# Kernel optimization log

Measured on AMD Instinct MI355X. Metric: run time of the kernel, lower is better.

Reference implementation:

```python
import jax, jax.numpy as jnp
import numpy as np

N_BITS = 8
OUTLIER_THRESHOLD = 3.0  # in units of per-token std
QMAX = 2.0 ** (N_BITS - 1) - 1.0  # 127 for int8
EPS = 1e-6


def setup_inputs() -> dict:
    key = jax.random.key(0)
    kx, kw, kb = jax.random.split(key, 3)
    B, S, D_in, D_out = 4, 4096, 2048, 2048
    x = jax.random.normal(kx, (B, S, D_in), dtype=jnp.float32)
    # nn.Linear default init scale ~ 1/sqrt(in_features)
    W = jax.random.normal(kw, (D_out, D_in), dtype=jnp.float32) / np.sqrt(D_in)
    b = jax.random.normal(kb, (D_out,), dtype=jnp.float32) / np.sqrt(D_in)
    return {"x": x, "W": W, "b": b}


def _dynamic_outlier_quant(y):
    # Per-token (last-dim) dynamic quantization with outlier awareness:
    #   1) outliers = values with |y| > threshold * std(token)
    #   2) inliers are fake-quantized to int8 with per-token absmax scale
    #      computed over the clamped (inlier) range
    #   3) outliers are kept at full precision
    std = jnp.std(y, axis=-1, keepdims=True)            # [B, S, 1]
    thr = OUTLIER_THRESHOLD * std
    outlier_mask = jnp.abs(y) > thr                      # [B, S, D]
    y_clamped = jnp.clip(y, -thr, thr)
    scale = jnp.max(jnp.abs(y_clamped), axis=-1, keepdims=True) / QMAX
    scale = jnp.maximum(scale, EPS)
    y_q = jnp.round(y_clamped / scale) * scale           # fake-quant inliers
    return jnp.where(outlier_mask, y, y_q)


def reference(x, W, b):
    # Linear: y = x @ W^T + b  -> [B, S, D_out]
    y = jnp.einsum("bsd,od->bso", x, W) + b
    return _dynamic_outlier_quant(y)
```

## Files before the change

kernel.cpp:

```cpp
#include <hip/hip_runtime.h>
#include <hip/hip_bf16.h>


typedef __attribute__((ext_vector_type(8))) short bf16x8;
typedef __attribute__((ext_vector_type(4))) float f32x4;
typedef __attribute__((ext_vector_type(8))) unsigned short u16x8;

#define QMAX_F 127.0f
#define THR_SIG 3.0f
#define EPS_F 1e-6f

__device__ __forceinline__ unsigned short f2bf(float f) {
    unsigned int u = __builtin_bit_cast(unsigned int, f);
    unsigned int r = u + 0x7fffu + ((u >> 16) & 1u);
    return (unsigned short)(r >> 16);
}

__device__ __forceinline__ void gl_lds16(const unsigned short* g, unsigned short* l) {
    __builtin_amdgcn_global_load_lds((const __attribute__((address_space(1))) void*)g,
                                     (__attribute__((address_space(3))) void*)l, 16, 0, 0);
}

__global__ __launch_bounds__(256) void k_convert2(const float* __restrict__ in0,
                                                  unsigned short* __restrict__ out0,
                                                  long long nA, int gA,
                                                  const float* __restrict__ in1,
                                                  unsigned short* __restrict__ out1,
                                                  long long nB) {
    const float* in;
    unsigned short* out;
    long long n, i;
    if (blockIdx.x < (unsigned)gA) {
        in = in0; out = out0; n = nA;
        i = ((long long)blockIdx.x * 256 + threadIdx.x) * 8;
    } else {
        in = in1; out = out1; n = nB;
        i = ((long long)(blockIdx.x - gA) * 256 + threadIdx.x) * 8;
    }
    if (i + 8 <= n) {
        f32x4 a = *(const f32x4*)(in + i);
        f32x4 b = *(const f32x4*)(in + i + 4);
        u16x8 o;
#pragma unroll
        for (int j = 0; j < 4; ++j) { o[j] = f2bf(a[j]); o[4 + j] = f2bf(b[j]); }
        *(u16x8*)(out + i) = o;
    }
}

#define STGA(h, i, tt)                                                              \
    gl_lds16(aSrc + (size_t)((h) * 128 + (i) * 64) * K + (tt) * 64,                 \
             &lds[((tt) & 1) * 32768 + (h) * 8192 + (i) * 4096 + dstW])
#define STGB(h, i, tt)                                                              \
    gl_lds16(bSrc + (size_t)((h) * 128 + (i) * 64) * K + (tt) * 64,                 \
             &lds[((tt) & 1) * 32768 + 16384 + (h) * 8192 + (i) * 4096 + dstW])

__global__ __launch_bounds__(512, 2) void k_gemm8(const unsigned short* __restrict__ A,
                                                  const unsigned short* __restrict__ B,
                                                  const float* __restrict__ bias,
                                                  float* __restrict__ C,
                                                  int M, int N, int K) {
    __shared__ unsigned short lds[65536];

    const int nbn = N >> 8;
    const int nwg = gridDim.x;
    int lin = blockIdx.x;
    int swz = lin;
    if ((nwg & 7) == 0) {
        int cpx = nwg >> 3;
        swz = (lin & 7) * cpx + (lin >> 3);
    }
    const int bm = swz / nbn, bn = swz % nbn;
    const int rowBase = bm << 8, colBase = bn << 8;

    const int tid = threadIdx.x;
    const int lane = tid & 63, w = tid >> 6;
    const int wr = w >> 2, wc = w & 3;

    const int lrow = lane >> 3;
    const int lslot = (lane & 7) ^ lrow;
    const unsigned short* aSrc = A + (size_t)(rowBase + w * 8 + lrow) * K + lslot * 8;
    const unsigned short* bSrc = B + (size_t)(colBase + w * 8 + lrow) * K + lslot * 8;
    const int dstW = w * 512;

    const int fr = lane & 15;
    const int ps0 = (((lane >> 4) ^ (lane & 7))) * 8;
    const int aO0 = wr * 8192 + fr * 64 + ps0;
    const int aO1 = wr * 8192 + fr * 64 + (ps0 ^ 32);
    const int bO0 = (wc >> 1) * 8192 + ((wc & 1) * 64 + fr) * 64 + ps0;
    const int bO1 = (wc >> 1) * 8192 + ((wc & 1) * 64 + fr) * 64 + (ps0 ^ 32);

    f32x4 acc[8][4];
#pragma unroll
    for (int i = 0; i < 8; ++i)
#pragma unroll
        for (int j = 0; j < 4; ++j) acc[i][j] = (f32x4){0.f, 0.f, 0.f, 0.f};

    const int nt = K >> 6;

    STGA(0, 0, 0); STGA(0, 1, 0); STGA(1, 0, 0); STGA(1, 1, 0);
    STGB(0, 0, 0); STGB(0, 1, 0); STGB(1, 0, 0); STGB(1, 1, 0);
    STGB(0, 0, 1); STGB(0, 1, 1); STGB(1, 0, 1); STGB(1, 1, 1);
    asm volatile("s_waitcnt vmcnt(4)" ::: "memory");
    __builtin_amdgcn_sched_barrier(0);
    __builtin_amdgcn_s_barrier();

    for (int t = 0; t < nt; ++t) {
        const unsigned short* Ab = lds + (t & 1) * 32768;
        const unsigned short* Bb = Ab + 16384;
        bf16x8 aQ[8], bLo[4], bHi[4];

#pragma unroll
        for (int mi = 0; mi < 4; ++mi) {
            aQ[2 * mi] = *(const bf16x8*)(Ab + aO0 + mi * 1024);
            aQ[2 * mi + 1] = *(const bf16x8*)(Ab + aO1 + mi * 1024);
        }
#pragma unroll
        for (int ni = 0; ni < 2; ++ni) {
            bLo[2 * ni] = *(const bf16x8*)(Bb + bO0 + ni * 1024);
            bLo[2 * ni + 1] = *(const bf16x8*)(Bb + bO1 + ni * 1024);
        }
        if (t + 1 < nt) { STGA(0, 0, t + 1); STGA(0, 1, t + 1); }
        __builtin_amdgcn_s_setprio(1);
#pragma unroll
        for (int mi = 0; mi < 4; ++mi)
#pragma unroll
            for (int ni = 0; ni < 2; ++ni) {
                acc[mi][ni] = __builtin_amdgcn_mfma_f32_16x16x32_bf16(
                    aQ[2 * mi], bLo[2 * ni], acc[mi][ni], 0, 0, 0);
                acc[mi][ni] = __builtin_amdgcn_mfma_f32_16x16x32_bf16(
                    aQ[2 * mi + 1], bLo[2 * ni + 1], acc[mi][ni], 0, 0, 0);
            }
        __builtin_amdgcn_s_setprio(0);
        __builtin_amdgcn_sched_barrier(0);
        __builtin_amdgcn_s_barrier();

#pragma unroll
        for (int ni = 0; ni < 2; ++ni) {
            bHi[2 * ni] = *(const bf16x8*)(Bb + bO0 + (ni + 2) * 1024);
            bHi[2 * ni + 1] = *(const bf16x8*)(Bb + bO1 + (ni + 2) * 1024);
        }
        if (t + 1 < nt) { STGA(1, 0, t + 1); STGA(1, 1, t + 1); }
        __builtin_amdgcn_s_setprio(1);
#pragma unroll
        for (int mi = 0; mi < 4; ++mi)
#pragma unroll
            for (int ni = 0; ni < 2; ++ni) {
                acc[mi][2 + ni] = __builtin_amdgcn_mfma_f32_16x16x32_bf16(
                    aQ[2 * mi], bHi[2 * ni], acc[mi][2 + ni], 0, 0, 0);
                acc[mi][2 + ni] = __builtin_amdgcn_mfma_f32_16x16x32_bf16(
                    aQ[2 * mi + 1], bHi[2 * ni + 1], acc[mi][2 + ni], 0, 0, 0);
            }
        __builtin_amdgcn_s_setprio(0);
        __builtin_amdgcn_sched_barrier(0);
        __builtin_amdgcn_s_barrier();

#pragma unroll
        for (int mi = 0; mi < 4; ++mi) {
            aQ[2 * mi] = *(const bf16x8*)(Ab + aO0 + (mi + 4) * 1024);
            aQ[2 * mi + 1] = *(const bf16x8*)(Ab + aO1 + (mi + 4) * 1024);
        }
        if (t + 2 < nt) { STGB(0, 0, t + 2); STGB(0, 1, t + 2); }
        __builtin_amdgcn_s_setprio(1);
#pragma unroll
        for (int mi = 0; mi < 4; ++mi)
#pragma unroll
            for (int ni = 0; ni < 2; ++ni) {
                acc[4 + mi][2 + ni] = __builtin_amdgcn_mfma_f32_16x16x32_bf16(
                    aQ[2 * mi], bHi[2 * ni], acc[4 + mi][2 + ni], 0, 0, 0);
                acc[4 + mi][2 + ni] = __builtin_amdgcn_mfma_f32_16x16x32_bf16(
                    aQ[2 * mi + 1], bHi[2 * ni + 1], acc[4 + mi][2 + ni], 0, 0, 0);
            }
        __builtin_amdgcn_s_setprio(0);
        __builtin_amdgcn_sched_barrier(0);
        __builtin_amdgcn_s_barrier();

        if (t + 2 < nt) { STGB(1, 0, t + 2); STGB(1, 1, t + 2); }
        __builtin_amdgcn_s_setprio(1);
#pragma unroll
        for (int mi = 0; mi < 4; ++mi)
#pragma unroll
            for (int ni = 0; ni < 2; ++ni) {
                acc[4 + mi][ni] = __builtin_amdgcn_mfma_f32_16x16x32_bf16(
                    aQ[2 * mi], bLo[2 * ni], acc[4 + mi][ni], 0, 0, 0);
                acc[4 + mi][ni] = __builtin_amdgcn_mfma_f32_16x16x32_bf16(
                    aQ[2 * mi + 1], bLo[2 * ni + 1], acc[4 + mi][ni], 0, 0, 0);
            }
        __builtin_amdgcn_s_setprio(0);
        __builtin_amdgcn_sched_barrier(0);
        if (t < nt - 2) {
            asm volatile("s_waitcnt vmcnt(4)" ::: "memory");
        } else {
            asm volatile("s_waitcnt vmcnt(0)" ::: "memory");
        }
        __builtin_amdgcn_sched_barrier(0);
        __builtin_amdgcn_s_barrier();
    }

    const int rowoff = (lane >> 4) * 4;
#pragma unroll
    for (int ni = 0; ni < 4; ++ni) {
        int gc = colBase + wc * 64 + ni * 16 + fr;
        float bv = bias[gc];
#pragma unroll
        for (int mi = 0; mi < 8; ++mi) {
            int gr = rowBase + wr * 128 + mi * 16 + rowoff;
#pragma unroll
            for (int r = 0; r < 4; ++r)
                C[(size_t)(gr + r) * N + gc] = acc[mi][ni][r] + bv;
        }
    }
}

__global__ __launch_bounds__(256) void k_gemm_f32(const float* __restrict__ Av,
                                                  const float* __restrict__ Bv,
                                                  const float* __restrict__ bias,
                                                  float* __restrict__ C,
                                                  int M, int N, int K) {
    __shared__ unsigned short sA[128 * 40];
    __shared__ unsigned short sB[128 * 40];

    const int nbn = N / 128;
    const int nwg = gridDim.x;
    int lin = blockIdx.x;
    int swz = lin;
    if ((nwg & 7) == 0) {
        int cpx = nwg >> 3;
        swz = (lin & 7) * cpx + (lin >> 3);
    }
    const int bm = swz / nbn, bn = swz % nbn;
    const int rowBase = bm * 128, colBase = bn * 128;

    const int tid = threadIdx.x;
    const int lane = tid & 63, wave = tid >> 6;
    const int wr = wave >> 1, wc = wave & 1;
    const int fr = lane & 15;
    const int kblk = (lane >> 4) * 8;

    f32x4 acc[4][4];
#pragma unroll
    for (int i = 0; i < 4; ++i)
#pragma unroll
        for (int j = 0; j < 4; ++j) acc[i][j] = (f32x4){0.f, 0.f, 0.f, 0.f};

    const int nk = K / 32;
    for (int kt = 0; kt < nk; ++kt) {
        const int kb = kt * 32;
        __syncthreads();
#pragma unroll
        for (int cc = 0; cc < 2; ++cc) {
            int c = tid + cc * 256;
            int row = c >> 2;
            int k8 = (c & 3) * 8;
            const float* gA = Av + (size_t)(rowBase + row) * K + kb + k8;
            const float* gB = Bv + (size_t)(colBase + row) * K + kb + k8;
            f32x4 a0 = *(const f32x4*)gA, a1 = *(const f32x4*)(gA + 4);
            f32x4 b0 = *(const f32x4*)gB, b1 = *(const f32x4*)(gB + 4);
            u16x8 va, vb;
#pragma unroll
            for (int j = 0; j < 4; ++j) {
                va[j] = f2bf(a0[j]); va[4 + j] = f2bf(a1[j]);
                vb[j] = f2bf(b0[j]); vb[4 + j] = f2bf(b1[j]);
            }
            *(u16x8*)&sA[row * 40 + k8] = va;
            *(u16x8*)&sB[row * 40 + k8] = vb;
        }
        __syncthreads();

        bf16x8 af[4], bfrag[4];
#pragma unroll
        for (int mi = 0; mi < 4; ++mi)
            af[mi] = *(const bf16x8*)&sA[(wr * 64 + mi * 16 + fr) * 40 + kblk];
#pragma unroll
        for (int ni = 0; ni < 4; ++ni)
            bfrag[ni] = *(const bf16x8*)&sB[(wc * 64 + ni * 16 + fr) * 40 + kblk];
#pragma unroll
        for (int mi = 0; mi < 4; ++mi)
#pragma unroll
            for (int ni = 0; ni < 4; ++ni)
                acc[mi][ni] = __builtin_amdgcn_mfma_f32_16x16x32_bf16(
                    af[mi], bfrag[ni], acc[mi][ni], 0, 0, 0);
    }

    const int rowoff = (lane >> 4) * 4;
#pragma unroll
    for (int ni = 0; ni < 4; ++ni) {
        int gc = colBase + wc * 64 + ni * 16 + fr;
        float bv = bias[gc];
#pragma unroll
        for (int mi = 0; mi < 4; ++mi) {
            int gr = rowBase + wr * 64 + mi * 16 + rowoff;
#pragma unroll
            for (int r = 0; r < 4; ++r)
                C[(size_t)(gr + r) * N + gc] = acc[mi][ni][r] + bv;
        }
    }
}

__global__ __launch_bounds__(256) void k_quant(float* __restrict__ y, int D) {
    float* p = y + (size_t)blockIdx.x * D;
    const int tid = threadIdx.x;
    f32x4 v0 = *(const f32x4*)(p + tid * 8);
    f32x4 v1 = *(const f32x4*)(p + tid * 8 + 4);

    float s = 0.f, ss = 0.f;
#pragma unroll
    for (int j = 0; j < 4; ++j) {
        s += v0[j] + v1[j];
        ss += v0[j] * v0[j] + v1[j] * v1[j];
    }
#pragma unroll
    for (int off = 32; off > 0; off >>= 1) {
        s += __shfl_down(s, off, 64);
        ss += __shfl_down(ss, off, 64);
    }

    __shared__ float rs[4], rss[4], bc[2];
    const int wave = tid >> 6, lane = tid & 63;
    if (lane == 0) { rs[wave] = s; rss[wave] = ss; }
    __syncthreads();
    if (tid == 0) {
        float S = rs[0] + rs[1] + rs[2] + rs[3];
        float SS = rss[0] + rss[1] + rss[2] + rss[3];
        float mean = S / (float)D;
        float var = fmaxf(SS / (float)D - mean * mean, 0.f);
        bc[0] = THR_SIG * sqrtf(var);
    }
    __syncthreads();
    const float thr = bc[0];

    float m = 0.f;
#pragma unroll
    for (int j = 0; j < 4; ++j) {
        m = fmaxf(m, fminf(fabsf(v0[j]), thr));
        m = fmaxf(m, fminf(fabsf(v1[j]), thr));
    }
#pragma unroll
    for (int off = 32; off > 0; off >>= 1) m = fmaxf(m, __shfl_down(m, off, 64));
    if (lane == 0) rs[wave] = m;
    __syncthreads();
    if (tid == 0) {
        float mm = fmaxf(fmaxf(rs[0], rs[1]), fmaxf(rs[2], rs[3]));
        bc[1] = fmaxf(mm / QMAX_F, EPS_F);
    }
    __syncthreads();
    const float scale = bc[1];

#pragma unroll
    for (int j = 0; j < 4; ++j) {
        {
            float v = v0[j];
            float c = fminf(fmaxf(v, -thr), thr);
            float q = rintf(c / scale) * scale;
            v0[j] = (fabsf(v) > thr) ? v : q;
        }
        {
            float v = v1[j];
            float c = fminf(fmaxf(v, -thr), thr);
            float q = rintf(c / scale) * scale;
            v1[j] = (fabsf(v) > thr) ? v : q;
        }
    }
    *(f32x4*)(p + tid * 8) = v0;
    *(f32x4*)(p + tid * 8 + 4) = v1;
}

extern "C" void kernel_launch(void* const* d_in, const int* in_sizes, int n_in,
                              void* d_out, int out_size, void* d_ws, size_t ws_size,
                              hipStream_t stream) {
    const float* x = (const float*)d_in[0];
    const float* W = (const float*)d_in[1];
    const float* b = (const float*)d_in[2];
    float* out = (float*)d_out;

    const int Dout = in_sizes[2];
    const int Din = in_sizes[1] / Dout;
    const int M = in_sizes[0] / Din;

    const size_t nA = (size_t)M * Din;
    const size_t nB = (size_t)Dout * Din;
    const size_t need = (nA + nB) * sizeof(unsigned short);
    const bool fits8 = (M % 256 == 0) && (Dout % 256 == 0) && (Din % 64 == 0) && (Din >= 256);
    const bool pre = (ws_size >= need) && fits8;

    if (pre) {
        unsigned short* xb = (unsigned short*)d_ws;
        unsigned short* wb = xb + nA;
        int gA = (int)((nA + 8 * 256 - 1) / (8 * 256));
        int gB = (int)((nB + 8 * 256 - 1) / (8 * 256));
        k_convert2<<<gA + gB, 256, 0, stream>>>(x, xb, (long long)nA, gA, W, wb, (long long)nB);
        int gridGemm = (M / 256) * (Dout / 256);
        k_gemm8<<<gridGemm, 512, 0, stream>>>(xb, wb, b, out, M, Dout, Din);
    } else {
        int gridGemm = (M / 128) * (Dout / 128);
        k_gemm_f32<<<gridGemm, 256, 0, stream>>>(x, W, b, out, M, Dout, Din);
    }
    k_quant<<<M, 256, 0, stream>>>(out, Dout);
}
```

Baseline: 203.8 us.

## Store GEMM output as bf16 in 4-row interleaved layout and quantize four rows per block

The GEMM epilogue now adds the bias, rounds to bf16 and writes groups of four consecutive rows interleaved as u16x4 into a workspace buffer. A new quant kernel reads this buffer, handles four tokens per block with vectorized reductions, and writes the fp32 result. This halves the bytes for the intermediate write and read between the two kernels. In exchange, the intermediate values, including the outliers that should stay at full precision, are rounded to bf16, which adds error. It also needs extra workspace and only applies when Dout is 2048.

```diff
diff --git a/kernel.cpp b/kernel.cpp
--- a/kernel.cpp
+++ b/kernel.cpp
@@ -5,6 +5,7 @@
 typedef __attribute__((ext_vector_type(8))) short bf16x8;
 typedef __attribute__((ext_vector_type(4))) float f32x4;
 typedef __attribute__((ext_vector_type(8))) unsigned short u16x8;
+typedef __attribute__((ext_vector_type(4))) unsigned short u16x4;
 
 #define QMAX_F 127.0f
 #define THR_SIG 3.0f
@@ -14,6 +15,10 @@
     unsigned int u = __builtin_bit_cast(unsigned int, f);
     unsigned int r = u + 0x7fffu + ((u >> 16) & 1u);
     return (unsigned short)(r >> 16);
+}
+
+__device__ __forceinline__ float bf2f(unsigned short h) {
+    return __builtin_bit_cast(float, (unsigned int)h << 16);
 }
 
 __device__ __forceinline__ void gl_lds16(const unsigned short* g, unsigned short* l) {
@@ -54,10 +59,12 @@
     gl_lds16(bSrc + (size_t)((h) * 128 + (i) * 64) * K + (tt) * 64,                 \
              &lds[((tt) & 1) * 32768 + 16384 + (h) * 8192 + (i) * 4096 + dstW])
 
+template <bool TILEOUT>
 __global__ __launch_bounds__(512, 2) void k_gemm8(const unsigned short* __restrict__ A,
                                                   const unsigned short* __restrict__ B,
                                                   const float* __restrict__ bias,
                                                   float* __restrict__ C,
+                                                  u16x4* __restrict__ C4,
                                                   int M, int N, int K) {
     __shared__ unsigned short lds[65536];
 
@@ -196,19 +203,115 @@
         __builtin_amdgcn_s_barrier();
     }
 
-    const int rowoff = (lane >> 4) * 4;
-#pragma unroll
-    for (int ni = 0; ni < 4; ++ni) {
-        int gc = colBase + wc * 64 + ni * 16 + fr;
-        float bv = bias[gc];
-#pragma unroll
-        for (int mi = 0; mi < 8; ++mi) {
-            int gr = rowBase + wr * 128 + mi * 16 + rowoff;
-#pragma unroll
-            for (int r = 0; r < 4; ++r)
-                C[(size_t)(gr + r) * N + gc] = acc[mi][ni][r] + bv;
-        }
-    }
+    if (TILEOUT) {
+        const int gr4base = (rowBase + wr * 128) >> 2;
+#pragma unroll
+        for (int ni = 0; ni < 4; ++ni) {
+            int gc = colBase + wc * 64 + ni * 16 + fr;
+            float bv = bias[gc];
+#pragma unroll
+            for (int mi = 0; mi < 8; ++mi) {
+                int gr4 = gr4base + mi * 4 + (lane >> 4);
+                u16x4 o;
+#pragma unroll
+                for (int r = 0; r < 4; ++r) o[r] = f2bf(acc[mi][ni][r] + bv);
+                C4[(size_t)gr4 * N + gc] = o;
+            }
+        }
+    } else {
+        const int rowoff = (lane >> 4) * 4;
+#pragma unroll
+        for (int ni = 0; ni < 4; ++ni) {
+            int gc = colBase + wc * 64 + ni * 16 + fr;
+            float bv = bias[gc];
+#pragma unroll
+            for (int mi = 0; mi < 8; ++mi) {
+                int gr = rowBase + wr * 128 + mi * 16 + rowoff;
+#pragma unroll
+                for (int r = 0; r < 4; ++r)
+                    C[(size_t)(gr + r) * N + gc] = acc[mi][ni][r] + bv;
+            }
+        }
+    }
+}
+
+__global__ __launch_bounds__(256) void k_quant4(const u16x4* __restrict__ Cp,
+                                                float* __restrict__ out, int D) {
+    constexpr int CH = 8;
+    const int g = blockIdx.x, t = threadIdx.x;
+    const u16x4* row = Cp + (size_t)g * D;
+
+    f32x4 y[CH];
+    f32x4 s = (f32x4){0.f, 0.f, 0.f, 0.f}, ss = s;
+#pragma unroll
+    for (int i = 0; i < CH; ++i) {
+        u16x4 v = row[i * 256 + t];
+#pragma unroll
+        for (int j = 0; j < 4; ++j) y[i][j] = bf2f(v[j]);
+        s += y[i];
+        ss += y[i] * y[i];
+    }
+#pragma unroll
+    for (int off = 32; off > 0; off >>= 1)
+#pragma unroll
+        for (int j = 0; j < 4; ++j) {
+            s[j] += __shfl_down(s[j], off, 64);
+            ss[j] += __shfl_down(ss[j], off, 64);
+        }
+
+    __shared__ f32x4 rs[4], rss[4], bc[2];
+    const int wave = t >> 6, lane = t & 63;
+    if (lane == 0) { rs[wave] = s; rss[wave] = ss; }
+    __syncthreads();
+    if (t == 0) {
+        f32x4 S = rs[0] + rs[1] + rs[2] + rs[3];
+        f32x4 SS = rss[0] + rss[1] + rss[2] + rss[3];
+        f32x4 thr;
+#pragma unroll
+        for (int j = 0; j < 4; ++j) {
+            float mean = S[j] / (float)2048;
+            float var = fmaxf(SS[j] / (float)2048 - mean * mean, 0.f);
+            thr[j] = THR_SIG * sqrtf(var);
+        }
+        bc[0] = thr;
+    }
+    __syncthreads();
+    const f32x4 thr = bc[0];
+
+    f32x4 m = (f32x4){0.f, 0.f, 0.f, 0.f};
+#pragma unroll
+    for (int i = 0; i < CH; ++i)
+#pragma unroll
+        for (int j = 0; j < 4; ++j)
+            m[j] = fmaxf(m[j], fminf(fabsf(y[i][j]), thr[j]));
+#pragma unroll
+    for (int off = 32; off > 0; off >>= 1)
+#pragma unroll
+        for (int j = 0; j < 4; ++j) m[j] = fmaxf(m[j], __shfl_down(m[j], off, 64));
+    if (lane == 0) rs[wave] = m;
+    __syncthreads();
+    if (t == 0) {
+        f32x4 sc;
+#pragma unroll
+        for (int j = 0; j < 4; ++j) {
+            float mm = fmaxf(fmaxf(rs[0][j], rs[1][j]), fmaxf(rs[2][j], rs[3][j]));
+            sc[j] = fmaxf(mm / QMAX_F, EPS_F);
+        }
+        bc[1] = sc;
+    }
+    __syncthreads();
+    const f32x4 scale = bc[1];
+
+#pragma unroll
+    for (int i = 0; i < CH; ++i)
+#pragma unroll
+        for (int j = 0; j < 4; ++j) {
+            float v = y[i][j];
+            float c = fminf(fmaxf(v, -thr[j]), thr[j]);
+            float q = rintf(c / scale[j]) * scale[j];
+            float res = (fabsf(v) > thr[j]) ? v : q;
+            out[(size_t)(g * 4 + j) * D + i * 256 + t] = res;
+        }
 }
 
 __global__ __launch_bounds__(256) void k_gemm_f32(const float* __restrict__ Av,
@@ -379,8 +482,10 @@
     const size_t nA = (size_t)M * Din;
     const size_t nB = (size_t)Dout * Din;
     const size_t need = (nA + nB) * sizeof(unsigned short);
+    const size_t need2 = need + (size_t)M * Dout * sizeof(unsigned short);
     const bool fits8 = (M % 256 == 0) && (Dout % 256 == 0) && (Din % 64 == 0) && (Din >= 256);
     const bool pre = (ws_size >= need) && fits8;
+    const bool pre2 = pre && (ws_size >= need2) && (Dout == 2048) && (M % 4 == 0);
 
     if (pre) {
         unsigned short* xb = (unsigned short*)d_ws;
@@ -389,10 +494,17 @@
         int gB = (int)((nB + 8 * 256 - 1) / (8 * 256));
         k_convert2<<<gA + gB, 256, 0, stream>>>(x, xb, (long long)nA, gA, W, wb, (long long)nB);
         int gridGemm = (M / 256) * (Dout / 256);
-        k_gemm8<<<gridGemm, 512, 0, stream>>>(xb, wb, b, out, M, Dout, Din);
+        if (pre2) {
+            u16x4* C4 = (u16x4*)(wb + nB);
+            k_gemm8<true><<<gridGemm, 512, 0, stream>>>(xb, wb, b, nullptr, C4, M, Dout, Din);
+            k_quant4<<<M / 4, 256, 0, stream>>>(C4, out, Dout);
+        } else {
+            k_gemm8<false><<<gridGemm, 512, 0, stream>>>(xb, wb, b, out, nullptr, M, Dout, Din);
+            k_quant<<<M, 256, 0, stream>>>(out, Dout);
+        }
     } else {
         int gridGemm = (M / 128) * (Dout / 128);
         k_gemm_f32<<<gridGemm, 256, 0, stream>>>(x, W, b, out, M, Dout, Din);
-    }
-    k_quant<<<M, 256, 0, stream>>>(out, Dout);
-}
+        k_quant<<<M, 256, 0, stream>>>(out, Dout);
+    }
+}
```

Result: faster. 194.1 us (-4.7%).
